# Kernel tuning notes

Measured on AMD Instinct MI355X. Metric: run time of the kernel, lower is better.

## Reference

```python
import jax, jax.numpy as jnp
import numpy as np

B, T, C = 256, 1024, 128
D = C // 2          # split_len1 == split_len2 == 64
CLAMP = 5.0


def setup_inputs() -> dict:
    key = jax.random.key(0)
    ks = jax.random.split(key, 13)
    p = lambda k, s: jax.random.normal(k, s, dtype=jnp.float32) * 0.1
    inp = {"x": jax.random.normal(ks[0], (B, T, C), dtype=jnp.float32)}
    for i, name in enumerate(["s1", "s2"]):
        b = 1 + i * 6
        inp[name + "_Wx"] = p(ks[b], (D, 3 * D))
        inp[name + "_Wh"] = p(ks[b + 1], (D, 3 * D))
        inp[name + "_bx"] = p(ks[b + 2], (3 * D,))
        inp[name + "_bh"] = p(ks[b + 3], (3 * D,))
        inp[name + "_Wo"] = p(ks[b + 4], (D, 2 * D))
        inp[name + "_bo"] = p(ks[b + 5], (2 * D,))
    return inp


def _gru(x, h, Wx, Wh, bx, bh, Wo, bo):
    # GRU cell with hidden size == input size, plus output projection (F_GRU).
    gx = x @ Wx + bx
    gh = h @ Wh + bh
    rx, zx, nx = jnp.split(gx, 3, axis=-1)
    rh, zh, nh = jnp.split(gh, 3, axis=-1)
    r = jax.nn.sigmoid(rx + rh)
    z = jax.nn.sigmoid(zx + zh)
    n = jnp.tanh(nx + r * nh)
    h_next = (1.0 - z) * n + z * h
    return h_next @ Wo + bo, h_next


def _e(s):
    # exp(clamp * 0.636 * atan(s / clamp)) -- soft-clamped scale
    return jnp.exp(CLAMP * 0.636 * jnp.arctan(s / CLAMP))


def reference(x, s1_Wx, s1_Wh, s1_bx, s1_bh, s1_Wo, s1_bo,
              s2_Wx, s2_Wh, s2_bx, s2_bh, s2_Wo, s2_bo):
    def step(carry, x_t):
        h1, h2 = carry
        x1, x2 = x_t[:, :D], x_t[:, D:]
        r2, h2n = _gru(x2, h2, s2_Wx, s2_Wh, s2_bx, s2_bh, s2_Wo, s2_bo)
        s2v, t2 = r2[:, :D], r2[:, D:]
        y1 = _e(s2v) * x1 + t2
        r1, h1n = _gru(y1, h1, s1_Wx, s1_Wh, s1_bx, s1_bh, s1_Wo, s1_bo)
        s1v, t1 = r1[:, :D], r1[:, D:]
        y2 = _e(s1v) * x2 + t1
        return (h1n, h2n), jnp.concatenate([y1, y2], axis=-1)

    h0 = (jnp.zeros((x.shape[0], D), x.dtype), jnp.zeros((x.shape[0], D), x.dtype))
    _, ys = jax.lax.scan(step, h0, jnp.swapaxes(x, 0, 1))  # scan over T
    return jnp.swapaxes(ys, 0, 1)  # [B, T, C]
```

## Files before the change

### kernel.cpp

```cpp
#include <hip/hip_runtime.h>

#define NB 256
#define NT 1024
#define NC 128
#define ND 64

typedef _Float16 f16x8 __attribute__((ext_vector_type(8)));
typedef float f32x4 __attribute__((ext_vector_type(4)));

__device__ __forceinline__ float fexp2(float x){
#if __has_builtin(__builtin_amdgcn_exp2f)
  return __builtin_amdgcn_exp2f(x);
#else
  return exp2f(x);
#endif
}
__device__ __forceinline__ float frcp_(float x){
#if __has_builtin(__builtin_amdgcn_rcpf)
  return __builtin_amdgcn_rcpf(x);
#else
  return 1.0f / x;
#endif
}
__device__ __forceinline__ float sigmoid_f(float x){
  return frcp_(1.0f + fexp2(-1.4426950408889634f * x));
}
__device__ __forceinline__ float tanh_f(float x){
  return 1.0f - 2.0f * frcp_(fexp2(2.8853900817779268f * x) + 1.0f);
}
__device__ __forceinline__ float e_func(float s){
  float u = 0.2f * s;
  float au = fabsf(u);
  bool inv = au > 1.0f;
  float v = inv ? frcp_(au) : au;
  float v2 = v * v;
  float pp = -0.0117212f;
  pp = pp * v2 + 0.05265332f;
  pp = pp * v2 - 0.11643287f;
  pp = pp * v2 + 0.19354346f;
  pp = pp * v2 - 0.33262347f;
  pp = pp * v2 + 0.99997726f;
  float at = pp * v;
  if (inv) at = 1.5707963267948966f - at;
  at = __builtin_copysignf(at, u);
  return fexp2(4.5877702301963f * at);
}

#define BAR() asm volatile("s_waitcnt lgkmcnt(0)\n\ts_barrier" ::: "memory")

__device__ __forceinline__ f16x8 ldaf(const _Float16* pack, int lane, int ks){
  return *reinterpret_cast<const f16x8*>(
      reinterpret_cast<const char*>(pack) + 16*(lane>>4) + 64*ks);
}
__device__ __forceinline__ f16x8 bld(const float* __restrict__ W, int ldw,
                                     int ks, int tile, int lane){
  f16x8 v;
  const int kb = ks*32 + 8*(lane>>4);
  const int c  = tile*16 + (lane&15);
  #pragma unroll
  for (int j = 0; j < 8; ++j) v[j] = (_Float16)W[(kb + j)*ldw + c];
  return v;
}
__device__ __forceinline__ float sel4(float a0, float a1, float a2, float a3, int lane){
  float t01 = (lane & 16) ? a1 : a0;
  float t23 = (lane & 16) ? a3 : a2;
  return (lane & 32) ? t23 : t01;
}
#define MFMA16(acc, a, bfr) acc = __builtin_amdgcn_mfma_f32_16x16x32_f16(a, bfr, acc, 0, 0, 0)

__global__ __launch_bounds__(384, 1)
void glow_gru_kernel(const float* __restrict__ x,
                     const float* __restrict__ Wx1, const float* __restrict__ Wh1,
                     const float* __restrict__ bx1, const float* __restrict__ bh1,
                     const float* __restrict__ Wo1, const float* __restrict__ bo1,
                     const float* __restrict__ Wx2, const float* __restrict__ Wh2,
                     const float* __restrict__ bx2, const float* __restrict__ bh2,
                     const float* __restrict__ Wo2, const float* __restrict__ bo2,
                     float* __restrict__ out)
{
  __shared__ __align__(16) _Float16 x2p[8][64];
  __shared__ __align__(16) _Float16 h2p[8][64];
  __shared__ __align__(16) _Float16 y1p[8][64];
  __shared__ __align__(16) _Float16 h1p[8][64];
  __shared__ float px2[8][192];
  __shared__ float py1[8][192];

  const int l = threadIdx.x;
  const int w = l >> 6;
  const int i = l & 63;
  const int b = blockIdx.x;
  const long xbase = (long)b * NT * NC;

  if (l < 64){ h2p[7][l] = (_Float16)0.f; h1p[7][l] = (_Float16)0.f; }

  if (w == 0){
    f16x8 bf[12][2];
    #pragma unroll
    for (int t = 0; t < 12; ++t){ bf[t][0] = bld(Wx2,192,0,t,i); bf[t][1] = bld(Wx2,192,1,t,i); }
    float xg[4], xn[4];
    #pragma unroll
    for (int s = 0; s < 4; ++s){
      x2p[s][i] = (_Float16)x[xbase + (long)s*NC + 64 + i];
      xg[s] = x[xbase + (long)(4+s)*NC + 64 + i];
    }
    __syncthreads();
    for (int J = 0; J <= 260; ++J){
      const int t0 = 4*J;
      #pragma unroll
      for (int s = 0; s < 4; ++s){
        const int tt = 4*(J+2) + s;
        xn[s] = (tt < NT) ? x[xbase + (long)tt*NC + 64 + i] : 0.f;
      }
      if (t0 < NT){
        f16x8 af[4][2];
        #pragma unroll
        for (int s = 0; s < 4; ++s){
          af[s][0] = ldaf(x2p[(t0+s)&7], i, 0);
          af[s][1] = ldaf(x2p[(t0+s)&7], i, 1);
        }
        #pragma unroll
        for (int s = 0; s < 4; ++s){
          f32x4 acc[12];
          #pragma unroll
          for (int t2 = 0; t2 < 12; ++t2){
            acc[t2] = (f32x4)0.f;
            MFMA16(acc[t2], af[s][0], bf[t2][0]);
            MFMA16(acc[t2], af[s][1], bf[t2][1]);
          }
          if (i < 16){
            #pragma unroll
            for (int t2 = 0; t2 < 12; ++t2) px2[(t0+s)&7][t2*16 + i] = acc[t2][0];
          }
        }
        const int tn0 = 4*(J+1);
        if (tn0 < NT){
          #pragma unroll
          for (int s = 0; s < 4; ++s) x2p[(tn0+s)&7][i] = (_Float16)xg[s];
        }
        #pragma unroll
        for (int s = 0; s < 4; ++s) xg[s] = xn[s];
      }
      BAR();
    }
  } else if (w == 1){
    f16x8 bf[12][2];
    #pragma unroll
    for (int t = 0; t < 12; ++t){ bf[t][0] = bld(Wx1,192,0,t,i); bf[t][1] = bld(Wx1,192,1,t,i); }
    __syncthreads();
    for (int J = 0; J <= 260; ++J){
      const int t0 = 4*(J-3);
      if (t0 >= 0 && t0 < NT){
        f16x8 af[4][2];
        #pragma unroll
        for (int s = 0; s < 4; ++s){
          af[s][0] = ldaf(y1p[(t0+s)&7], i, 0);
          af[s][1] = ldaf(y1p[(t0+s)&7], i, 1);
        }
        #pragma unroll
        for (int s = 0; s < 4; ++s){
          f32x4 acc[12];
          #pragma unroll
          for (int t2 = 0; t2 < 12; ++t2){
            acc[t2] = (f32x4)0.f;
            MFMA16(acc[t2], af[s][0], bf[t2][0]);
            MFMA16(acc[t2], af[s][1], bf[t2][1]);
          }
          if (i < 16){
            #pragma unroll
            for (int t2 = 0; t2 < 12; ++t2) py1[(t0+s)&7][t2*16 + i] = acc[t2][0];
          }
        }
      }
      BAR();
    }
  } else if (w == 2 || w == 3){
    const bool isA = (w == 2);
    const float* WH = isA ? Wh2 : Wh1;
    const float* bx = isA ? bx2 : bx1;
    const float* bh = isA ? bh2 : bh1;
    _Float16 (*hr)[64] = isA ? h2p : h1p;
    float (*pr)[192]   = isA ? px2 : py1;
    const int lag = isA ? 1 : 4;
    f16x8 bf[12][2];
    #pragma unroll
    for (int t = 0; t < 12; ++t){ bf[t][0] = bld(WH,192,0,t,i); bf[t][1] = bld(WH,192,1,t,i); }
    const float b0 = bx[i] + bh[i];
    const float b1 = bx[64+i] + bh[64+i];
    const float b2v = bx[128+i], b3v = bh[128+i];
    float h = 0.f;
    __syncthreads();
    for (int J = 0; J <= 260; ++J){
      const int t0 = 4*(J - lag);
      if (t0 >= 0 && t0 < NT){
        float rxs[4], zxs[4], nxs[4];
        #pragma unroll
        for (int s = 0; s < 4; ++s){
          rxs[s] = pr[(t0+s)&7][i];
          zxs[s] = pr[(t0+s)&7][64+i];
          nxs[s] = pr[(t0+s)&7][128+i];
        }
        #pragma unroll
        for (int s = 0; s < 4; ++s){
          const int t = t0 + s;
          f16x8 a0 = ldaf(hr[(t-1)&7], i, 0);
          f16x8 a1 = ldaf(hr[(t-1)&7], i, 1);
          f32x4 acc[12];
          #pragma unroll
          for (int t2 = 0; t2 < 12; ++t2){
            acc[t2] = (f32x4)0.f;
            MFMA16(acc[t2], a0, bf[t2][0]);
            MFMA16(acc[t2], a1, bf[t2][1]);
          }
          float rh = sel4(acc[0][0], acc[1][0], acc[2][0],  acc[3][0],  i);
          float zh = sel4(acc[4][0], acc[5][0], acc[6][0],  acc[7][0],  i);
          float nh = sel4(acc[8][0], acc[9][0], acc[10][0], acc[11][0], i);
          float r = sigmoid_f(rxs[s] + rh + b0);
          float z = sigmoid_f(zxs[s] + zh + b1);
          float nn = tanh_f(nxs[s] + b2v + r*(nh + b3v));
          h = (1.f - z)*nn + z*h;
          hr[t&7][i] = (_Float16)h;
        }
      }
      BAR();
    }
  } else {
    const bool isB = (w == 4);
    const float* WO = isB ? Wo2 : Wo1;
    const float* bo = isB ? bo2 : bo1;
    _Float16 (*hr)[64] = isB ? h2p : h1p;
    const int lag  = isB ? 2 : 5;
    const int xoff = isB ? 0 : 64;
    f16x8 bf[8][2];
    #pragma unroll
    for (int t = 0; t < 8; ++t){ bf[t][0] = bld(WO,128,0,t,i); bf[t][1] = bld(WO,128,1,t,i); }
    const float b0 = bo[i], b1 = bo[64+i];
    float xg[4], xn[4];
    #pragma unroll
    for (int s = 0; s < 4; ++s) xg[s] = x[xbase + (long)s*NC + xoff + i];
    __syncthreads();
    for (int J = 0; J <= 260; ++J){
      const int t0 = 4*(J - lag);
      #pragma unroll
      for (int s = 0; s < 4; ++s){
        const int tt = 4*(J - lag + 1) + s;
        xn[s] = (tt >= 0 && tt < NT) ? x[xbase + (long)tt*NC + xoff + i] : 0.f;
      }
      if (t0 >= 0 && t0 < NT){
        f16x8 af[4][2];
        #pragma unroll
        for (int s = 0; s < 4; ++s){
          af[s][0] = ldaf(hr[(t0+s)&7], i, 0);
          af[s][1] = ldaf(hr[(t0+s)&7], i, 1);
        }
        #pragma unroll
        for (int s = 0; s < 4; ++s){
          const int t = t0 + s;
          f32x4 acc[8];
          #pragma unroll
          for (int t2 = 0; t2 < 8; ++t2){
            acc[t2] = (f32x4)0.f;
            MFMA16(acc[t2], af[s][0], bf[t2][0]);
            MFMA16(acc[t2], af[s][1], bf[t2][1]);
          }
          float sv = sel4(acc[0][0], acc[1][0], acc[2][0], acc[3][0], i);
          float tv = sel4(acc[4][0], acc[5][0], acc[6][0], acc[7][0], i);
          float y = e_func(sv + b0) * xg[s] + (tv + b1);
          out[xbase + (long)t*NC + xoff + i] = y;
          if (isB) y1p[t&7][i] = (_Float16)y;
        }
        #pragma unroll
        for (int s = 0; s < 4; ++s) xg[s] = xn[s];
      }
      BAR();
    }
  }
}

extern "C" void kernel_launch(void* const* d_in, const int* in_sizes, int n_in,
                              void* d_out, int out_size, void* d_ws, size_t ws_size,
                              hipStream_t stream) {
  const float* x   = (const float*)d_in[0];
  const float* Wx1 = (const float*)d_in[1];
  const float* Wh1 = (const float*)d_in[2];
  const float* bx1 = (const float*)d_in[3];
  const float* bh1 = (const float*)d_in[4];
  const float* Wo1 = (const float*)d_in[5];
  const float* bo1 = (const float*)d_in[6];
  const float* Wx2 = (const float*)d_in[7];
  const float* Wh2 = (const float*)d_in[8];
  const float* bx2 = (const float*)d_in[9];
  const float* bh2 = (const float*)d_in[10];
  const float* Wo2 = (const float*)d_in[11];
  const float* bo2 = (const float*)d_in[12];
  float* out = (float*)d_out;

  hipLaunchKernelGGL(glow_gru_kernel, dim3(NB), dim3(384), 0, stream,
                     x, Wx1, Wh1, bx1, bh1, Wo1, bo1,
                     Wx2, Wh2, bx2, bh2, Wo2, bo2, out);
}
```

Baseline: 440.8 us.

## Double pipeline stage width and pass GRU hidden state through lane permutes

Each pipeline stage now covers 8 timesteps instead of 4, which halves the number of block-wide barriers. The shared-memory ring buffers grow to 16 slots to match. The recurrent GRU warps no longer read the previous hidden state back from LDS. They rebuild the MFMA A-operand in registers with ds_swizzle and ds_bpermute, which shortens the serial dependency chain per step. The block grows to 8 waves: the recurrent wave moves to wave 6 and wave 7 only takes part in barriers. This adds idle waves and register pressure.

```diff
diff --git a/kernel.cpp b/kernel.cpp
--- a/kernel.cpp
+++ b/kernel.cpp
@@ -4,6 +4,9 @@
 #define NT 1024
 #define NC 128
 #define ND 64
+#define SP 8
+#define NSL 16
+#define NJ 132
 
 typedef _Float16 f16x8 __attribute__((ext_vector_type(8)));
 typedef float f32x4 __attribute__((ext_vector_type(4)));
@@ -68,7 +71,23 @@
 }
 #define MFMA16(acc, a, bfr) acc = __builtin_amdgcn_mfma_f32_16x16x32_f16(a, bfr, acc, 0, 0, 0)
 
-__global__ __launch_bounds__(384, 1)
+__device__ __forceinline__ void redist(float h, int lane, const int* addrs,
+                                       f16x8* a0, f16x8* a1){
+  int hswi = __builtin_amdgcn_ds_swizzle(__builtin_bit_cast(int, h), 0x041F);
+  float hsw = __builtin_bit_cast(float, hswi);
+  float lo = (lane & 1) ? hsw : h;
+  float hp = (lane & 1) ? h : hsw;
+  int pd = __builtin_bit_cast(int, __builtin_amdgcn_cvt_pkrtz(lo, hp));
+  int d[8];
+  #pragma unroll
+  for (int q = 0; q < 8; ++q) d[q] = __builtin_amdgcn_ds_bpermute(addrs[q], pd);
+  union { int u[4]; f16x8 v; } u0, u1;
+  u0.u[0]=d[0]; u0.u[1]=d[1]; u0.u[2]=d[2]; u0.u[3]=d[3];
+  u1.u[0]=d[4]; u1.u[1]=d[5]; u1.u[2]=d[6]; u1.u[3]=d[7];
+  *a0 = u0.v; *a1 = u1.v;
+}
+
+__global__ __launch_bounds__(512, 1)
 void glow_gru_kernel(const float* __restrict__ x,
                      const float* __restrict__ Wx1, const float* __restrict__ Wh1,
                      const float* __restrict__ bx1, const float* __restrict__ bh1,
@@ -78,12 +97,12 @@
                      const float* __restrict__ Wo2, const float* __restrict__ bo2,
                      float* __restrict__ out)
 {
-  __shared__ __align__(16) _Float16 x2p[8][64];
-  __shared__ __align__(16) _Float16 h2p[8][64];
-  __shared__ __align__(16) _Float16 y1p[8][64];
-  __shared__ __align__(16) _Float16 h1p[8][64];
-  __shared__ float px2[8][192];
-  __shared__ float py1[8][192];
+  __shared__ __align__(16) _Float16 x2p[NSL][64];
+  __shared__ __align__(16) _Float16 h2p[NSL][64];
+  __shared__ __align__(16) _Float16 y1p[NSL][64];
+  __shared__ __align__(16) _Float16 h1p[NSL][64];
+  __shared__ float px2[NSL][192];
+  __shared__ float py1[NSL][192];
 
   const int l = threadIdx.x;
   const int w = l >> 6;
@@ -91,54 +110,48 @@
   const int b = blockIdx.x;
   const long xbase = (long)b * NT * NC;
 
-  if (l < 64){ h2p[7][l] = (_Float16)0.f; h1p[7][l] = (_Float16)0.f; }
-
   if (w == 0){
     f16x8 bf[12][2];
     #pragma unroll
     for (int t = 0; t < 12; ++t){ bf[t][0] = bld(Wx2,192,0,t,i); bf[t][1] = bld(Wx2,192,1,t,i); }
-    float xg[4], xn[4];
-    #pragma unroll
-    for (int s = 0; s < 4; ++s){
+    float xg[SP], xn[SP];
+    #pragma unroll
+    for (int s = 0; s < SP; ++s){
       x2p[s][i] = (_Float16)x[xbase + (long)s*NC + 64 + i];
-      xg[s] = x[xbase + (long)(4+s)*NC + 64 + i];
-    }
-    __syncthreads();
-    for (int J = 0; J <= 260; ++J){
-      const int t0 = 4*J;
+      xg[s] = x[xbase + (long)(SP+s)*NC + 64 + i];
+    }
+    __syncthreads();
+    for (int J = 0; J <= NJ; ++J){
+      const int t0 = SP*J;
       #pragma unroll
-      for (int s = 0; s < 4; ++s){
-        const int tt = 4*(J+2) + s;
+      for (int s = 0; s < SP; ++s){
+        const int tt = SP*(J+2) + s;
         xn[s] = (tt < NT) ? x[xbase + (long)tt*NC + 64 + i] : 0.f;
       }
       if (t0 < NT){
-        f16x8 af[4][2];
-        #pragma unroll
-        for (int s = 0; s < 4; ++s){
-          af[s][0] = ldaf(x2p[(t0+s)&7], i, 0);
-          af[s][1] = ldaf(x2p[(t0+s)&7], i, 1);
-        }
-        #pragma unroll
-        for (int s = 0; s < 4; ++s){
+        #pragma unroll
+        for (int s = 0; s < SP; ++s){
+          const int t = t0 + s;
+          f16x8 a0 = ldaf(x2p[t&(NSL-1)], i, 0);
+          f16x8 a1 = ldaf(x2p[t&(NSL-1)], i, 1);
           f32x4 acc[12];
-          #pragma unroll
-          for (int t2 = 0; t2 < 12; ++t2){
-            acc[t2] = (f32x4)0.f;
-            MFMA16(acc[t2], af[s][0], bf[t2][0]);
-            MFMA16(acc[t2], af[s][1], bf[t2][1]);
-          }
+          f32x4 zz = {0.f,0.f,0.f,0.f};
+          #pragma unroll
+          for (int t2 = 0; t2 < 12; ++t2){ acc[t2] = zz; MFMA16(acc[t2], a0, bf[t2][0]); }
+          #pragma unroll
+          for (int t2 = 0; t2 < 12; ++t2){ MFMA16(acc[t2], a1, bf[t2][1]); }
           if (i < 16){
             #pragma unroll
-            for (int t2 = 0; t2 < 12; ++t2) px2[(t0+s)&7][t2*16 + i] = acc[t2][0];
+            for (int t2 = 0; t2 < 12; ++t2) px2[t&(NSL-1)][t2*16 + i] = acc[t2][0];
           }
         }
-        const int tn0 = 4*(J+1);
+        const int tn0 = SP*(J+1);
         if (tn0 < NT){
           #pragma unroll
-          for (int s = 0; s < 4; ++s) x2p[(tn0+s)&7][i] = (_Float16)xg[s];
-        }
-        #pragma unroll
-        for (int s = 0; s < 4; ++s) xg[s] = xn[s];
+          for (int s = 0; s < SP; ++s) x2p[(tn0+s)&(NSL-1)][i] = (_Float16)xg[s];
+        }
+        #pragma unroll
+        for (int s = 0; s < SP; ++s) xg[s] = xn[s];
       }
       BAR();
     }
@@ -147,33 +160,29 @@
     #pragma unroll
     for (int t = 0; t < 12; ++t){ bf[t][0] = bld(Wx1,192,0,t,i); bf[t][1] = bld(Wx1,192,1,t,i); }
     __syncthreads();
-    for (int J = 0; J <= 260; ++J){
-      const int t0 = 4*(J-3);
+    for (int J = 0; J <= NJ; ++J){
+      const int t0 = SP*(J-3);
       if (t0 >= 0 && t0 < NT){
-        f16x8 af[4][2];
-        #pragma unroll
-        for (int s = 0; s < 4; ++s){
-          af[s][0] = ldaf(y1p[(t0+s)&7], i, 0);
-          af[s][1] = ldaf(y1p[(t0+s)&7], i, 1);
-        }
-        #pragma unroll
-        for (int s = 0; s < 4; ++s){
+        #pragma unroll
+        for (int s = 0; s < SP; ++s){
+          const int t = t0 + s;
+          f16x8 a0 = ldaf(y1p[t&(NSL-1)], i, 0);
+          f16x8 a1 = ldaf(y1p[t&(NSL-1)], i, 1);
           f32x4 acc[12];
-          #pragma unroll
-          for (int t2 = 0; t2 < 12; ++t2){
-            acc[t2] = (f32x4)0.f;
-            MFMA16(acc[t2], af[s][0], bf[t2][0]);
-            MFMA16(acc[t2], af[s][1], bf[t2][1]);
-          }
+          f32x4 zz = {0.f,0.f,0.f,0.f};
+          #pragma unroll
+          for (int t2 = 0; t2 < 12; ++t2){ acc[t2] = zz; MFMA16(acc[t2], a0, bf[t2][0]); }
+          #pragma unroll
+          for (int t2 = 0; t2 < 12; ++t2){ MFMA16(acc[t2], a1, bf[t2][1]); }
           if (i < 16){
             #pragma unroll
-            for (int t2 = 0; t2 < 12; ++t2) py1[(t0+s)&7][t2*16 + i] = acc[t2][0];
+            for (int t2 = 0; t2 < 12; ++t2) py1[t&(NSL-1)][t2*16 + i] = acc[t2][0];
           }
         }
       }
       BAR();
     }
-  } else if (w == 2 || w == 3){
+  } else if (w == 2 || w == 6){
     const bool isA = (w == 2);
     const float* WH = isA ? Wh2 : Wh1;
     const float* bx = isA ? bx2 : bx1;
@@ -184,33 +193,35 @@
     f16x8 bf[12][2];
     #pragma unroll
     for (int t = 0; t < 12; ++t){ bf[t][0] = bld(WH,192,0,t,i); bf[t][1] = bld(WH,192,1,t,i); }
+    int addrs[8];
+    #pragma unroll
+    for (int q = 0; q < 8; ++q) addrs[q] = 8*(16*(q>>2) + 4*(i>>4) + (q&3));
     const float b0 = bx[i] + bh[i];
     const float b1 = bx[64+i] + bh[64+i];
     const float b2v = bx[128+i], b3v = bh[128+i];
     float h = 0.f;
     __syncthreads();
-    for (int J = 0; J <= 260; ++J){
-      const int t0 = 4*(J - lag);
+    for (int J = 0; J <= NJ; ++J){
+      const int t0 = SP*(J - lag);
       if (t0 >= 0 && t0 < NT){
-        float rxs[4], zxs[4], nxs[4];
-        #pragma unroll
-        for (int s = 0; s < 4; ++s){
-          rxs[s] = pr[(t0+s)&7][i];
-          zxs[s] = pr[(t0+s)&7][64+i];
-          nxs[s] = pr[(t0+s)&7][128+i];
-        }
-        #pragma unroll
-        for (int s = 0; s < 4; ++s){
+        float rxs[SP], zxs[SP], nxs[SP];
+        #pragma unroll
+        for (int s = 0; s < SP; ++s){
+          rxs[s] = pr[(t0+s)&(NSL-1)][i];
+          zxs[s] = pr[(t0+s)&(NSL-1)][64+i];
+          nxs[s] = pr[(t0+s)&(NSL-1)][128+i];
+        }
+        #pragma unroll
+        for (int s = 0; s < SP; ++s){
           const int t = t0 + s;
-          f16x8 a0 = ldaf(hr[(t-1)&7], i, 0);
-          f16x8 a1 = ldaf(hr[(t-1)&7], i, 1);
+          f16x8 a0, a1;
+          redist(h, i, addrs, &a0, &a1);
           f32x4 acc[12];
-          #pragma unroll
-          for (int t2 = 0; t2 < 12; ++t2){
-            acc[t2] = (f32x4)0.f;
-            MFMA16(acc[t2], a0, bf[t2][0]);
-            MFMA16(acc[t2], a1, bf[t2][1]);
-          }
+          f32x4 zz = {0.f,0.f,0.f,0.f};
+          #pragma unroll
+          for (int t2 = 0; t2 < 12; ++t2){ acc[t2] = zz; MFMA16(acc[t2], a0, bf[t2][0]); }
+          #pragma unroll
+          for (int t2 = 0; t2 < 12; ++t2){ MFMA16(acc[t2], a1, bf[t2][1]); }
           float rh = sel4(acc[0][0], acc[1][0], acc[2][0],  acc[3][0],  i);
           float zh = sel4(acc[4][0], acc[5][0], acc[6][0],  acc[7][0],  i);
           float nh = sel4(acc[8][0], acc[9][0], acc[10][0], acc[11][0], i);
@@ -218,12 +229,12 @@
           float z = sigmoid_f(zxs[s] + zh + b1);
           float nn = tanh_f(nxs[s] + b2v + r*(nh + b3v));
           h = (1.f - z)*nn + z*h;
-          hr[t&7][i] = (_Float16)h;
+          hr[t&(NSL-1)][i] = (_Float16)h;
         }
       }
       BAR();
     }
-  } else {
+  } else if (w == 4 || w == 5){
     const bool isB = (w == 4);
     const float* WO = isB ? Wo2 : Wo1;
     const float* bo = isB ? bo2 : bo1;
@@ -234,45 +245,43 @@
     #pragma unroll
     for (int t = 0; t < 8; ++t){ bf[t][0] = bld(WO,128,0,t,i); bf[t][1] = bld(WO,128,1,t,i); }
     const float b0 = bo[i], b1 = bo[64+i];
-    float xg[4], xn[4];
-    #pragma unroll
-    for (int s = 0; s < 4; ++s) xg[s] = x[xbase + (long)s*NC + xoff + i];
-    __syncthreads();
-    for (int J = 0; J <= 260; ++J){
-      const int t0 = 4*(J - lag);
+    float xg[SP], xn[SP];
+    #pragma unroll
+    for (int s = 0; s < SP; ++s) xg[s] = x[xbase + (long)s*NC + xoff + i];
+    __syncthreads();
+    for (int J = 0; J <= NJ; ++J){
+      const int t0 = SP*(J - lag);
       #pragma unroll
-      for (int s = 0; s < 4; ++s){
-        const int tt = 4*(J - lag + 1) + s;
+      for (int s = 0; s < SP; ++s){
+        const int tt = t0 + SP + s;
         xn[s] = (tt >= 0 && tt < NT) ? x[xbase + (long)tt*NC + xoff + i] : 0.f;
       }
       if (t0 >= 0 && t0 < NT){
-        f16x8 af[4][2];
-        #pragma unroll
-        for (int s = 0; s < 4; ++s){
-          af[s][0] = ldaf(hr[(t0+s)&7], i, 0);
-          af[s][1] = ldaf(hr[(t0+s)&7], i, 1);
-        }
-        #pragma unroll
-        for (int s = 0; s < 4; ++s){
+        #pragma unroll
+        for (int s = 0; s < SP; ++s){
           const int t = t0 + s;
+          f16x8 a0 = ldaf(hr[t&(NSL-1)], i, 0);
+          f16x8 a1 = ldaf(hr[t&(NSL-1)], i, 1);
           f32x4 acc[8];
-          #pragma unroll
-          for (int t2 = 0; t2 < 8; ++t2){
-            acc[t2] = (f32x4)0.f;
-            MFMA16(acc[t2], af[s][0], bf[t2][0]);
-            MFMA16(acc[t2], af[s][1], bf[t2][1]);
-          }
+          f32x4 zz = {0.f,0.f,0.f,0.f};
+          #pragma unroll
+          for (int t2 = 0; t2 < 8; ++t2){ acc[t2] = zz; MFMA16(acc[t2], a0, bf[t2][0]); }
+          #pragma unroll
+          for (int t2 = 0; t2 < 8; ++t2){ MFMA16(acc[t2], a1, bf[t2][1]); }
           float sv = sel4(acc[0][0], acc[1][0], acc[2][0], acc[3][0], i);
           float tv = sel4(acc[4][0], acc[5][0], acc[6][0], acc[7][0], i);
           float y = e_func(sv + b0) * xg[s] + (tv + b1);
           out[xbase + (long)t*NC + xoff + i] = y;
-          if (isB) y1p[t&7][i] = (_Float16)y;
-        }
-        #pragma unroll
-        for (int s = 0; s < 4; ++s) xg[s] = xn[s];
+          if (isB) y1p[t&(NSL-1)][i] = (_Float16)y;
+        }
+        #pragma unroll
+        for (int s = 0; s < SP; ++s) xg[s] = xn[s];
       }
       BAR();
     }
+  } else {
+    __syncthreads();
+    for (int J = 0; J <= NJ; ++J){ BAR(); }
   }
 }
 
@@ -294,7 +303,7 @@
   const float* bo2 = (const float*)d_in[12];
   float* out = (float*)d_out;
 
-  hipLaunchKernelGGL(glow_gru_kernel, dim3(NB), dim3(384), 0, stream,
+  hipLaunchKernelGGL(glow_gru_kernel, dim3(NB), dim3(512), 0, stream,
                      x, Wx1, Wh1, bx1, bh1, Wo1, bo1,
                      Wx2, Wh2, bx2, bh2, Wo2, bo2, out);
 }
```

Result: slower. 541.9 us (+22.9%).
